# Kernel optimization log

Hardware: AMD Instinct MI355X
Metric: run time of the kernel (lower is better)

The kernel has to match this reference:

```python
import jax, jax.numpy as jnp
import numpy as np

B = 8192        # batch of CLIP image features
EMB = 512       # emb_dim / key_dim
POOL = 100      # pool_size (rows of key table and prompt pool)
TOP_K = 4
C_LEN = 8       # c_length; split in half into Ck / Cv
EPS = 1e-12     # torch F.normalize eps


def setup_inputs() -> dict:
    key = jax.random.key(0)
    k0, k1, k2, k3, k4 = jax.random.split(key, 5)
    return {
        "x_block": jax.random.normal(k0, (B, EMB), dtype=jnp.float32),
        "x_query": jax.random.normal(k1, (B, 1, EMB), dtype=jnp.float32),
        "clip_key": jax.random.normal(k2, (POOL, EMB), dtype=jnp.float32),
        "W": jax.random.normal(k3, (EMB, EMB), dtype=jnp.float32) * 0.02,
        "b": jnp.zeros((EMB,), dtype=jnp.float32),
        "c_pool": jax.random.normal(k4, (POOL, C_LEN, EMB), dtype=jnp.float32) * 0.02,
        "l": 2,
    }


def _l2_normalize(x, axis):
    n = jnp.sqrt(jnp.sum(x * x, axis=axis, keepdims=True))
    return x / jnp.maximum(n, EPS)


def reference(x_block, x_query, clip_key, W, b, c_pool, l):
    # l == 2 is in c_layers -> class-prompt path (g-layer path not exercised)
    xq = x_query[:, 0, :]                       # squeeze(1): [B, EMB]
    x = jax.nn.relu(xq @ W.T + b)               # forward_ffn
    q = _l2_normalize(x, axis=1)                # [B, EMB]
    n_K = _l2_normalize(clip_key, axis=1)       # [POOL, EMB]
    cos_sim = jnp.einsum('bj,kj->bk', q, n_K)   # [B, POOL]
    _, idx = jax.lax.top_k(cos_sim, TOP_K)      # [B, TOP_K]
    P = c_pool[idx]                             # gather: [B, TOP_K, C_LEN, EMB]
    half = C_LEN // 2
    Ck = P[:, :, :half, :].reshape(B, TOP_K * half, EMB)
    Cv = P[:, :, half:, :].reshape(B, TOP_K * half, EMB)
    return (Ck, Cv, x_block)
```

## Files before the change

kernel.cpp:

```cpp
#include <hip/hip_runtime.h>
#include <math.h>

#define NB    8192
#define EMB   512
#define POOL  100

#define BM    32
#define BN    256
#define BK    64
#define AS_STRIDE 36
#define XT_STRIDE 516
#define BS_STRIDE 260
#define KS_STRIDE 104
#define SC_STRIDE 101

__global__ __launch_bounds__(64) void key_norms_k(const float* __restrict__ K,
                                                  float* __restrict__ inv) {
    const int key  = blockIdx.x;
    const int lane = threadIdx.x;
    const float4* row = (const float4*)(K + (size_t)key * EMB);
    float4 v0 = row[lane];
    float4 v1 = row[lane + 64];
    float s = v0.x*v0.x + v0.y*v0.y + v0.z*v0.z + v0.w*v0.w
            + v1.x*v1.x + v1.y*v1.y + v1.z*v1.z + v1.w*v1.w;
    #pragma unroll
    for (int off = 32; off > 0; off >>= 1) s += __shfl_xor(s, off);
    if (lane == 0) inv[key] = 1.0f / fmaxf(sqrtf(s), 1e-12f);
}

__global__ __launch_bounds__(512) void fused_score_topk_k(
    const float* __restrict__ xq,
    const float* __restrict__ W,
    const float* __restrict__ bias,
    const float* __restrict__ Kc,
    const float* __restrict__ inv,
    int* __restrict__ idx_out)
{
    __shared__ float xt[BM * XT_STRIDE];
    __shared__ float As[BK * AS_STRIDE];
    __shared__ float ubuf[BK * BS_STRIDE];

    const int tid = threadIdx.x;
    const int r0  = blockIdx.x * BM;
    const int rt  = tid >> 6;
    const int ct  = tid & 63;

    for (int jt = 0; jt < EMB; jt += BN) {
        float acc[4][4];
        #pragma unroll
        for (int i = 0; i < 4; ++i)
            #pragma unroll
            for (int q = 0; q < 4; ++q) acc[i][q] = 0.f;

        for (int kt = 0; kt < EMB; kt += BK) {
            {
                int r  = tid >> 4;
                int kq = (tid & 15) << 2;
                float4 v = *(const float4*)(xq + (size_t)(r0 + r) * EMB + kt + kq);
                As[(kq+0)*AS_STRIDE + r] = v.x;
                As[(kq+1)*AS_STRIDE + r] = v.y;
                As[(kq+2)*AS_STRIDE + r] = v.z;
                As[(kq+3)*AS_STRIDE + r] = v.w;
            }
            #pragma unroll
            for (int i = 0; i < 8; ++i) {
                int u  = tid + (i << 9);
                int j  = u >> 4;
                int kq = (u & 15) << 2;
                float4 v = *(const float4*)(W + (size_t)(jt + j) * EMB + kt + kq);
                ubuf[(kq+0)*BS_STRIDE + j] = v.x;
                ubuf[(kq+1)*BS_STRIDE + j] = v.y;
                ubuf[(kq+2)*BS_STRIDE + j] = v.z;
                ubuf[(kq+3)*BS_STRIDE + j] = v.w;
            }
            __syncthreads();
            #pragma unroll 16
            for (int kk = 0; kk < BK; ++kk) {
                float4 a = *(const float4*)&As[kk*AS_STRIDE + (rt<<2)];
                float4 b = *(const float4*)&ubuf[kk*BS_STRIDE + (ct<<2)];
                acc[0][0] += a.x*b.x; acc[0][1] += a.x*b.y; acc[0][2] += a.x*b.z; acc[0][3] += a.x*b.w;
                acc[1][0] += a.y*b.x; acc[1][1] += a.y*b.y; acc[1][2] += a.y*b.z; acc[1][3] += a.y*b.w;
                acc[2][0] += a.z*b.x; acc[2][1] += a.z*b.y; acc[2][2] += a.z*b.z; acc[2][3] += a.z*b.w;
                acc[3][0] += a.w*b.x; acc[3][1] += a.w*b.y; acc[3][2] += a.w*b.z; acc[3][3] += a.w*b.w;
            }
            __syncthreads();
        }
        {
            float4 bv = *(const float4*)(bias + jt + (ct<<2));
            #pragma unroll
            for (int i = 0; i < 4; ++i) {
                int r = (rt<<2) + i;
                float4 o;
                o.x = fmaxf(acc[i][0] + bv.x, 0.f);
                o.y = fmaxf(acc[i][1] + bv.y, 0.f);
                o.z = fmaxf(acc[i][2] + bv.z, 0.f);
                o.w = fmaxf(acc[i][3] + bv.w, 0.f);
                *(float4*)&xt[r*XT_STRIDE + jt + (ct<<2)] = o;
            }
        }
    }
    __syncthreads();

    const int tr = tid >> 5;
    const int tc = tid & 31;
    float sacc[2][4] = {{0.f,0.f,0.f,0.f},{0.f,0.f,0.f,0.f}};
    for (int kt = 0; kt < EMB; kt += 32) {
        __syncthreads();
        for (int u = tid; u < 800; u += 512) {
            int key = u >> 3;
            int kq  = (u & 7) << 2;
            float iv = inv[key];
            float4 v = *(const float4*)(Kc + (size_t)key * EMB + kt + kq);
            ubuf[(kq+0)*KS_STRIDE + key] = v.x * iv;
            ubuf[(kq+1)*KS_STRIDE + key] = v.y * iv;
            ubuf[(kq+2)*KS_STRIDE + key] = v.z * iv;
            ubuf[(kq+3)*KS_STRIDE + key] = v.w * iv;
        }
        __syncthreads();
        if (tc < 25) {
            #pragma unroll
            for (int kk = 0; kk < 32; ++kk) {
                float a0 = xt[(tr<<1)*XT_STRIDE + kt + kk];
                float a1 = xt[((tr<<1)+1)*XT_STRIDE + kt + kk];
                float4 b = *(const float4*)&ubuf[kk*KS_STRIDE + (tc<<2)];
                sacc[0][0] += a0*b.x; sacc[0][1] += a0*b.y; sacc[0][2] += a0*b.z; sacc[0][3] += a0*b.w;
                sacc[1][0] += a1*b.x; sacc[1][1] += a1*b.y; sacc[1][2] += a1*b.z; sacc[1][3] += a1*b.w;
            }
        }
    }

    __syncthreads();
    if (tc < 25) {
        #pragma unroll
        for (int i = 0; i < 2; ++i)
            #pragma unroll
            for (int q = 0; q < 4; ++q)
                ubuf[((tr<<1)+i)*SC_STRIDE + (tc<<2) + q] = sacc[i][q];
    }
    __syncthreads();
    if (tid < BM) {
        const float* srow = &ubuf[tid * SC_STRIDE];
        float v0=-INFINITY, v1=-INFINITY, v2=-INFINITY, v3=-INFINITY;
        int   i0=0, i1=0, i2=0, i3=0;
        for (int j = 0; j < POOL; ++j) {
            float s = srow[j];
            if (s > v3) {
                if (s > v0)      { v3=v2;i3=i2; v2=v1;i2=i1; v1=v0;i1=i0; v0=s;i0=j; }
                else if (s > v1) { v3=v2;i3=i2; v2=v1;i2=i1; v1=s;i1=j; }
                else if (s > v2) { v3=v2;i3=i2; v2=s;i2=j; }
                else             { v3=s;i3=j; }
            }
        }
        int4 w; w.x=i0; w.y=i1; w.z=i2; w.w=i3;
        *(int4*)(idx_out + (size_t)(r0 + tid) * 4) = w;
    }
}

__global__ __launch_bounds__(256) void gather_k(
    const float* __restrict__ c_pool,
    const float* __restrict__ x_block,
    const int*   __restrict__ idx,
    float* __restrict__ out)
{
    const int b   = blockIdx.x;
    const int tid = threadIdx.x;
    const int F4  = EMB / 4;

    int4 id = *(const int4*)(idx + (size_t)b * 4);

    float4*       outCk = (float4*)out + (size_t)b * 16 * F4;
    float4*       outCv = (float4*)out + (size_t)NB * 16 * F4 + (size_t)b * 16 * F4;
    float4*       outX  = (float4*)out + (size_t)2 * NB * 16 * F4 + (size_t)b * F4;
    const float4* cp    = (const float4*)c_pool;
    const float4* xb    = (const float4*)x_block + (size_t)b * F4;

    #pragma unroll
    for (int t = 0; t < 4; ++t) {
        int id_t = (t == 0) ? id.x : (t == 1) ? id.y : (t == 2) ? id.z : id.w;
        const float4* src = cp + (size_t)(id_t * 8) * F4;
        #pragma unroll
        for (int i = 0; i < 2; ++i) {
            int u = tid + (i << 8);
            int c = u >> 7;
            int j = u & 127;
            outCk[(t*4 + c) * F4 + j] = src[c * F4 + j];
            outCv[(t*4 + c) * F4 + j] = src[(4 + c) * F4 + j];
        }
    }
    if (tid < F4) outX[tid] = xb[tid];
}

extern "C" void kernel_launch(void* const* d_in, const int* in_sizes, int n_in,
                              void* d_out, int out_size, void* d_ws, size_t ws_size,
                              hipStream_t stream) {
    (void)in_sizes; (void)n_in; (void)out_size; (void)ws_size;
    const float* x_block  = (const float*)d_in[0];
    const float* x_query  = (const float*)d_in[1];
    const float* clip_key = (const float*)d_in[2];
    const float* W        = (const float*)d_in[3];
    const float* bias     = (const float*)d_in[4];
    const float* c_pool   = (const float*)d_in[5];

    float* inv = (float*)d_ws;
    int*   idx = (int*)((char*)d_ws + 512);
    float* out = (float*)d_out;

    key_norms_k<<<POOL, 64, 0, stream>>>(clip_key, inv);
    fused_score_topk_k<<<NB / BM, 512, 0, stream>>>(x_query, W, bias, clip_key, inv, idx);
    gather_k<<<NB, 256, 0, stream>>>(c_pool, x_block, idx, out);
}
```

Baseline: 706.7 us.

## Fuse gather into score/top-k kernel with smaller tiles and nontemporal stores

Merges the prompt gather and x_block copy into the GEMM/score/top-k kernel, so indices stay in shared memory and the idx round trip plus a separate launch go away. The GEMM tile shrinks to 16 rows with BK 32 and 256 threads, and shared-memory tiles switch from transposed to row-major with float4 dot-product inner loops. Output writes use nontemporal stores to avoid polluting cache. Tradeoffs: each block serially writes 16 rows of gather output after its compute, and with twice as many blocks W is re-read from global memory more often.

```diff
diff --git a/kernel.cpp b/kernel.cpp
--- a/kernel.cpp
+++ b/kernel.cpp
@@ -5,14 +5,16 @@
 #define EMB   512
 #define POOL  100
 
-#define BM    32
+#define BM    16
 #define BN    256
-#define BK    64
-#define AS_STRIDE 36
-#define XT_STRIDE 516
-#define BS_STRIDE 260
-#define KS_STRIDE 104
-#define SC_STRIDE 101
+#define BK    32
+#define AS_S  36
+#define BS_S  36
+#define XT_S  516
+#define KS_S  100
+#define SC_S  101
+
+typedef float v4f __attribute__((ext_vector_type(4)));
 
 __global__ __launch_bounds__(64) void key_norms_k(const float* __restrict__ K,
                                                   float* __restrict__ inv) {
@@ -28,22 +30,26 @@
     if (lane == 0) inv[key] = 1.0f / fmaxf(sqrtf(s), 1e-12f);
 }
 
-__global__ __launch_bounds__(512) void fused_score_topk_k(
+__global__ __launch_bounds__(256, 2) void fused_all_k(
     const float* __restrict__ xq,
     const float* __restrict__ W,
     const float* __restrict__ bias,
     const float* __restrict__ Kc,
     const float* __restrict__ inv,
-    int* __restrict__ idx_out)
+    const float* __restrict__ c_pool,
+    const float* __restrict__ x_block,
+    float* __restrict__ out)
 {
-    __shared__ float xt[BM * XT_STRIDE];
-    __shared__ float As[BK * AS_STRIDE];
-    __shared__ float ubuf[BK * BS_STRIDE];
+    __shared__ float As[BM * AS_S];
+    __shared__ float Bs[BN * BS_S];
+    __shared__ float xt[BM * XT_S];
+    __shared__ int4  sIdx[BM];
 
     const int tid = threadIdx.x;
     const int r0  = blockIdx.x * BM;
-    const int rt  = tid >> 6;
-    const int ct  = tid & 63;
+
+    const int rt = tid >> 6;
+    const int ct = tid & 63;
 
     for (int jt = 0; jt < EMB; jt += BN) {
         float acc[4][4];
@@ -53,93 +59,92 @@
             for (int q = 0; q < 4; ++q) acc[i][q] = 0.f;
 
         for (int kt = 0; kt < EMB; kt += BK) {
-            {
-                int r  = tid >> 4;
-                int kq = (tid & 15) << 2;
+            __syncthreads();
+            if (tid < 128) {
+                int r  = tid >> 3;
+                int kq = (tid & 7) << 2;
                 float4 v = *(const float4*)(xq + (size_t)(r0 + r) * EMB + kt + kq);
-                As[(kq+0)*AS_STRIDE + r] = v.x;
-                As[(kq+1)*AS_STRIDE + r] = v.y;
-                As[(kq+2)*AS_STRIDE + r] = v.z;
-                As[(kq+3)*AS_STRIDE + r] = v.w;
+                *(float4*)&As[r * AS_S + kq] = v;
             }
             #pragma unroll
             for (int i = 0; i < 8; ++i) {
-                int u  = tid + (i << 9);
-                int j  = u >> 4;
-                int kq = (u & 15) << 2;
+                int u  = tid + (i << 8);
+                int j  = u >> 3;
+                int kq = (u & 7) << 2;
                 float4 v = *(const float4*)(W + (size_t)(jt + j) * EMB + kt + kq);
-                ubuf[(kq+0)*BS_STRIDE + j] = v.x;
-                ubuf[(kq+1)*BS_STRIDE + j] = v.y;
-                ubuf[(kq+2)*BS_STRIDE + j] = v.z;
-                ubuf[(kq+3)*BS_STRIDE + j] = v.w;
+                *(float4*)&Bs[j * BS_S + kq] = v;
             }
             __syncthreads();
-            #pragma unroll 16
-            for (int kk = 0; kk < BK; ++kk) {
-                float4 a = *(const float4*)&As[kk*AS_STRIDE + (rt<<2)];
-                float4 b = *(const float4*)&ubuf[kk*BS_STRIDE + (ct<<2)];
-                acc[0][0] += a.x*b.x; acc[0][1] += a.x*b.y; acc[0][2] += a.x*b.z; acc[0][3] += a.x*b.w;
-                acc[1][0] += a.y*b.x; acc[1][1] += a.y*b.y; acc[1][2] += a.y*b.z; acc[1][3] += a.y*b.w;
-                acc[2][0] += a.z*b.x; acc[2][1] += a.z*b.y; acc[2][2] += a.z*b.z; acc[2][3] += a.z*b.w;
-                acc[3][0] += a.w*b.x; acc[3][1] += a.w*b.y; acc[3][2] += a.w*b.z; acc[3][3] += a.w*b.w;
-            }
-            __syncthreads();
-        }
-        {
-            float4 bv = *(const float4*)(bias + jt + (ct<<2));
-            #pragma unroll
-            for (int i = 0; i < 4; ++i) {
-                int r = (rt<<2) + i;
-                float4 o;
-                o.x = fmaxf(acc[i][0] + bv.x, 0.f);
-                o.y = fmaxf(acc[i][1] + bv.y, 0.f);
-                o.z = fmaxf(acc[i][2] + bv.z, 0.f);
-                o.w = fmaxf(acc[i][3] + bv.w, 0.f);
-                *(float4*)&xt[r*XT_STRIDE + jt + (ct<<2)] = o;
-            }
-        }
-    }
-    __syncthreads();
+            #pragma unroll
+            for (int kk = 0; kk < BK; kk += 4) {
+                float4 a[4], b[4];
+                #pragma unroll
+                for (int i = 0; i < 4; ++i)
+                    a[i] = *(const float4*)&As[((rt << 2) + i) * AS_S + kk];
+                #pragma unroll
+                for (int q = 0; q < 4; ++q)
+                    b[q] = *(const float4*)&Bs[(ct + (q << 6)) * BS_S + kk];
+                #pragma unroll
+                for (int i = 0; i < 4; ++i)
+                    #pragma unroll
+                    for (int q = 0; q < 4; ++q)
+                        acc[i][q] += a[i].x*b[q].x + a[i].y*b[q].y
+                                   + a[i].z*b[q].z + a[i].w*b[q].w;
+            }
+        }
+        #pragma unroll
+        for (int q = 0; q < 4; ++q) {
+            float bq = bias[jt + ct + (q << 6)];
+            #pragma unroll
+            for (int i = 0; i < 4; ++i)
+                xt[((rt << 2) + i) * XT_S + jt + ct + (q << 6)]
+                    = fmaxf(acc[i][q] + bq, 0.f);
+        }
+    }
 
     const int tr = tid >> 5;
     const int tc = tid & 31;
+    float* Ks = Bs;
     float sacc[2][4] = {{0.f,0.f,0.f,0.f},{0.f,0.f,0.f,0.f}};
     for (int kt = 0; kt < EMB; kt += 32) {
         __syncthreads();
-        for (int u = tid; u < 800; u += 512) {
+        for (int u = tid; u < 800; u += 256) {
             int key = u >> 3;
             int kq  = (u & 7) << 2;
             float iv = inv[key];
             float4 v = *(const float4*)(Kc + (size_t)key * EMB + kt + kq);
-            ubuf[(kq+0)*KS_STRIDE + key] = v.x * iv;
-            ubuf[(kq+1)*KS_STRIDE + key] = v.y * iv;
-            ubuf[(kq+2)*KS_STRIDE + key] = v.z * iv;
-            ubuf[(kq+3)*KS_STRIDE + key] = v.w * iv;
+            Ks[(kq+0)*KS_S + key] = v.x * iv;
+            Ks[(kq+1)*KS_S + key] = v.y * iv;
+            Ks[(kq+2)*KS_S + key] = v.z * iv;
+            Ks[(kq+3)*KS_S + key] = v.w * iv;
         }
         __syncthreads();
         if (tc < 25) {
             #pragma unroll
             for (int kk = 0; kk < 32; ++kk) {
-                float a0 = xt[(tr<<1)*XT_STRIDE + kt + kk];
-                float a1 = xt[((tr<<1)+1)*XT_STRIDE + kt + kk];
-                float4 b = *(const float4*)&ubuf[kk*KS_STRIDE + (tc<<2)];
-                sacc[0][0] += a0*b.x; sacc[0][1] += a0*b.y; sacc[0][2] += a0*b.z; sacc[0][3] += a0*b.w;
-                sacc[1][0] += a1*b.x; sacc[1][1] += a1*b.y; sacc[1][2] += a1*b.z; sacc[1][3] += a1*b.w;
+                float a0 = xt[(tr << 1) * XT_S + kt + kk];
+                float a1 = xt[((tr << 1) + 1) * XT_S + kt + kk];
+                float4 b = *(const float4*)&Ks[kk * KS_S + (tc << 2)];
+                sacc[0][0] += a0*b.x; sacc[0][1] += a0*b.y;
+                sacc[0][2] += a0*b.z; sacc[0][3] += a0*b.w;
+                sacc[1][0] += a1*b.x; sacc[1][1] += a1*b.y;
+                sacc[1][2] += a1*b.z; sacc[1][3] += a1*b.w;
             }
         }
     }
 
     __syncthreads();
+    float* sc = Bs;
     if (tc < 25) {
         #pragma unroll
         for (int i = 0; i < 2; ++i)
             #pragma unroll
             for (int q = 0; q < 4; ++q)
-                ubuf[((tr<<1)+i)*SC_STRIDE + (tc<<2) + q] = sacc[i][q];
+                sc[((tr << 1) + i) * SC_S + (tc << 2) + q] = sacc[i][q];
     }
     __syncthreads();
     if (tid < BM) {
-        const float* srow = &ubuf[tid * SC_STRIDE];
+        const float* srow = &sc[tid * SC_S];
         float v0=-INFINITY, v1=-INFINITY, v2=-INFINITY, v3=-INFINITY;
         int   i0=0, i1=0, i2=0, i3=0;
         for (int j = 0; j < POOL; ++j) {
@@ -152,42 +157,44 @@
             }
         }
         int4 w; w.x=i0; w.y=i1; w.z=i2; w.w=i3;
-        *(int4*)(idx_out + (size_t)(r0 + tid) * 4) = w;
-    }
-}
-
-__global__ __launch_bounds__(256) void gather_k(
-    const float* __restrict__ c_pool,
-    const float* __restrict__ x_block,
-    const int*   __restrict__ idx,
-    float* __restrict__ out)
-{
-    const int b   = blockIdx.x;
-    const int tid = threadIdx.x;
-    const int F4  = EMB / 4;
-
-    int4 id = *(const int4*)(idx + (size_t)b * 4);
-
-    float4*       outCk = (float4*)out + (size_t)b * 16 * F4;
-    float4*       outCv = (float4*)out + (size_t)NB * 16 * F4 + (size_t)b * 16 * F4;
-    float4*       outX  = (float4*)out + (size_t)2 * NB * 16 * F4 + (size_t)b * F4;
-    const float4* cp    = (const float4*)c_pool;
-    const float4* xb    = (const float4*)x_block + (size_t)b * F4;
-
+        sIdx[tid] = w;
+    }
+    __syncthreads();
+
+    float4*       out4 = (float4*)out;
+    const float4* cp4  = (const float4*)c_pool;
+    const float4* xb4  = (const float4*)x_block;
+    const size_t  CV0  = (size_t)NB * 2048;
+    const size_t  X0   = (size_t)2 * NB * 2048;
+
+    for (int r = 0; r < BM; ++r) {
+        int4 id = sIdx[r];
+        int ids[4] = {id.x, id.y, id.z, id.w};
+        float4* oCk = out4 + (size_t)(r0 + r) * 2048;
+        float4* oCv = out4 + CV0 + (size_t)(r0 + r) * 2048;
+        #pragma unroll
+        for (int t = 0; t < 4; ++t) {
+            const float4* src = cp4 + (size_t)ids[t] * 1024;
+            #pragma unroll
+            for (int rep = 0; rep < 2; ++rep) {
+                int u = tid + (rep << 8);
+                int c = u >> 7;
+                int j = u & 127;
+                __builtin_nontemporal_store(*(const v4f*)&src[c * 128 + j],
+                                            (v4f*)&oCk[((t << 2) + c) * 128 + j]);
+                __builtin_nontemporal_store(*(const v4f*)&src[(c + 4) * 128 + j],
+                                            (v4f*)&oCv[((t << 2) + c) * 128 + j]);
+            }
+        }
+    }
     #pragma unroll
-    for (int t = 0; t < 4; ++t) {
-        int id_t = (t == 0) ? id.x : (t == 1) ? id.y : (t == 2) ? id.z : id.w;
-        const float4* src = cp + (size_t)(id_t * 8) * F4;
-        #pragma unroll
-        for (int i = 0; i < 2; ++i) {
-            int u = tid + (i << 8);
-            int c = u >> 7;
-            int j = u & 127;
-            outCk[(t*4 + c) * F4 + j] = src[c * F4 + j];
-            outCv[(t*4 + c) * F4 + j] = src[(4 + c) * F4 + j];
-        }
-    }
-    if (tid < F4) outX[tid] = xb[tid];
+    for (int rep = 0; rep < 8; ++rep) {
+        int u = tid + (rep << 8);
+        int r = u >> 7;
+        int j = u & 127;
+        __builtin_nontemporal_store(*(const v4f*)&xb4[(size_t)(r0 + r) * 128 + j],
+                                    (v4f*)&out4[X0 + (size_t)(r0 + r) * 128 + j]);
+    }
 }
 
 extern "C" void kernel_launch(void* const* d_in, const int* in_sizes, int n_in,
@@ -202,10 +209,9 @@
     const float* c_pool   = (const float*)d_in[5];
 
     float* inv = (float*)d_ws;
-    int*   idx = (int*)((char*)d_ws + 512);
     float* out = (float*)d_out;
 
     key_norms_k<<<POOL, 64, 0, stream>>>(clip_key, inv);
-    fused_score_topk_k<<<NB / BM, 512, 0, stream>>>(x_query, W, bias, clip_key, inv, idx);
-    gather_k<<<NB, 256, 0, stream>>>(c_pool, x_block, idx, out);
+    fused_all_k<<<NB / BM, 256, 0, stream>>>(x_query, W, bias, clip_key, inv,
+                                             c_pool, x_block, out);
 }
```

Result: no change. 698.1 us (-1.2%).
